# Kernel optimization log

Hardware: AMD Instinct MI355X
Metric: run time of the kernel (lower is better)

The kernel has to match this reference:

```python
import jax, jax.numpy as jnp
import numpy as np
from jax import lax

# Model dims (match init_kwargs / input_specs)
B, L, DIN, H = 8, 2048, 40, 128
NL, DSTATE, DCONV, EXPAND, DTRANK = 4, 16, 4, 2, 8
DINNER = EXPAND * H
NHOR, NCLS = 3, 3


def _layer_norm(x, g, b, eps=1e-5):
    m = jnp.mean(x, -1, keepdims=True)
    v = jnp.mean((x - m) ** 2, -1, keepdims=True)
    return (x - m) * lax.rsqrt(v + eps) * g + b


def _mamba_block(x, in_w, cw, cb, xp_w, dt_w, dt_b, A_log, Dp, out_w):
    # x: (b, l, H)
    b, l, _ = x.shape
    xz = x @ in_w.T                      # (b, l, 2*d_inner)
    xh, z = jnp.split(xz, 2, axis=-1)
    # causal depthwise conv1d (torch pads d_conv-1 both sides then slices [:l])
    xc = lax.conv_general_dilated(
        xh.transpose(0, 2, 1), cw, window_strides=(1,),
        padding=[(DCONV - 1, 0)], feature_group_count=DINNER,
        dimension_numbers=('NCH', 'OIH', 'NCH')) + cb[None, :, None]
    xh = jax.nn.silu(xc.transpose(0, 2, 1))   # (b, l, d_inner)
    # selective SSM
    A = -jnp.exp(A_log)                   # (N,)
    xp = xh @ xp_w.T                      # (b, l, dt_rank + 2N)
    dt_in, Bm, Cm = jnp.split(xp, [DTRANK, DTRANK + DSTATE], axis=-1)
    delta = jax.nn.softplus(dt_in @ dt_w.T + dt_b)          # (b, l, d_inner)
    dA = jnp.exp(delta[..., None] * A)                      # (b, l, d_inner, N)
    dBx = delta[..., None] * Bm[:, :, None, :] * xh[..., None]

    def step(h, inp):
        dA_t, dBx_t, C_t = inp
        h = dA_t * h + dBx_t              # (b, d_inner, N)
        y = jnp.einsum('bdn,bn->bd', h, C_t)
        return h, y

    h0 = jnp.zeros((b, DINNER, DSTATE), x.dtype)
    _, ys = lax.scan(step, h0, (dA.transpose(1, 0, 2, 3),
                                dBx.transpose(1, 0, 2, 3),
                                Cm.transpose(1, 0, 2)))
    y = ys.transpose(1, 0, 2) + Dp * xh   # (b, l, d_inner)
    y = y * jax.nn.silu(z)
    return y @ out_w.T                    # (b, l, H)


def _forward(x, input_proj_w, input_proj_b, input_norm_g, input_norm_b,
             norm_g, norm_b, in_proj_w, conv_w, conv_b, x_proj_w,
             dt_proj_w, dt_proj_b, A_log, D, out_proj_w,
             head_w1, head_b1, head_w2, head_b2):
    h = _layer_norm(x @ input_proj_w.T + input_proj_b, input_norm_g, input_norm_b)
    for i in range(NL):  # residual Mamba blocks (pre-norm)
        h = h + _mamba_block(_layer_norm(h, norm_g[i], norm_b[i]),
                             in_proj_w[i], conv_w[i], conv_b[i], x_proj_w[i],
                             dt_proj_w[i], dt_proj_b[i], A_log[i], D[i], out_proj_w[i])
    feats = h[:, -1, :]                   # last-timestep features (b, H)
    logits = []
    for i in range(NHOR):
        t = jax.nn.gelu(feats @ head_w1[i].T + head_b1[i], approximate=False)
        logits.append(t @ head_w2[i].T + head_b2[i])
    return jnp.stack(logits, axis=1)      # (b, num_horizons, num_classes)


def setup_inputs() -> dict:
    key = jax.random.key(0)
    ks = jax.random.split(key, 12)
    rn = lambda k, s, sc=0.02: jax.random.normal(k, s, jnp.float32) * sc
    A0 = jnp.log(jnp.arange(1, DSTATE + 1, dtype=jnp.float32))
    return {
        'x': jax.random.normal(ks[0], (B, L, DIN), jnp.float32),
        'input_proj_w': rn(ks[1], (H, DIN)),
        'input_proj_b': jnp.zeros((H,), jnp.float32),
        'input_norm_g': jnp.ones((H,), jnp.float32),
        'input_norm_b': jnp.zeros((H,), jnp.float32),
        'norm_g': jnp.ones((NL, H), jnp.float32),
        'norm_b': jnp.zeros((NL, H), jnp.float32),
        'in_proj_w': rn(ks[2], (NL, 2 * DINNER, H)),
        'conv_w': rn(ks[3], (NL, DINNER, 1, DCONV), 0.1),
        'conv_b': jnp.zeros((NL, DINNER), jnp.float32),
        'x_proj_w': rn(ks[4], (NL, DTRANK + 2 * DSTATE, DINNER)),
        'dt_proj_w': rn(ks[5], (NL, DINNER, DTRANK), 0.1),
        'dt_proj_b': rn(ks[6], (NL, DINNER), 0.1),
        'A_log': jnp.tile(A0, (NL, 1)),
        'D': jnp.ones((NL, DINNER), jnp.float32),
        'out_proj_w': rn(ks[7], (NL, H, DINNER)),
        'head_w1': rn(ks[8], (NHOR, H // 2, H)),
        'head_b1': jnp.zeros((NHOR, H // 2), jnp.float32),
        'head_w2': rn(ks[9], (NHOR, NCLS, H // 2)),
        'head_b2': jnp.zeros((NHOR, NCLS), jnp.float32),
    }


def reference(x, input_proj_w, input_proj_b, input_norm_g, input_norm_b,
              norm_g, norm_b, in_proj_w, conv_w, conv_b, x_proj_w,
              dt_proj_w, dt_proj_b, A_log, D, out_proj_w,
              head_w1, head_b1, head_w2, head_b2):
    return _forward(x, input_proj_w, input_proj_b, input_norm_g, input_norm_b,
                    norm_g, norm_b, in_proj_w, conv_w, conv_b, x_proj_w,
                    dt_proj_w, dt_proj_b, A_log, D, out_proj_w,
                    head_w1, head_b1, head_w2, head_b2)
```

## Files before the change

kernel.cpp:

```cpp
#include <hip/hip_runtime.h>
#include <hip/hip_bf16.h>
#include <math.h>

#define B_  8
#define L_  2048
#define DIN_ 40
#define H_  128
#define NL_ 4
#define DSTATE_ 16
#define DCONV_ 4
#define DTRANK_ 8
#define DINNER_ 256
#define NHOR_ 3
#define NCLS_ 3

#define CL_ 32
#define NC_ 64

__device__ __forceinline__ float softplus_f(float x) {
  return fmaxf(x, 0.f) + log1pf(__expf(-fabsf(x)));
}

__device__ __forceinline__ bool a_is_arith(const float* Ag, float& An0) {
  An0 = -__expf(Ag[0]);
  if (An0 == 0.f) return false;
  bool ok = true;
#pragma unroll
  for (int n = 1; n < DSTATE_; n++) {
    float r = -__expf(Ag[n]) / An0;
    ok = ok && (fabsf(r - (float)(n + 1)) < 1e-3f);
  }
  return ok;
}

__global__ __launch_bounds__(128) void k_in_ln(
    const float* __restrict__ x, const float* __restrict__ w,
    const float* __restrict__ bias, const float* __restrict__ g,
    const float* __restrict__ bb, float* __restrict__ hout)
{
  int row = blockIdx.x;
  int o = threadIdx.x;
  __shared__ float xs[DIN_];
  __shared__ float sm[4];
  if (o < DIN_) xs[o] = x[(size_t)row * DIN_ + o];
  __syncthreads();
  float acc = bias[o];
  const float* wr = w + (size_t)o * DIN_;
#pragma unroll
  for (int k = 0; k < DIN_; k++) acc += xs[k] * wr[k];
  float s = acc;
#pragma unroll
  for (int m = 32; m >= 1; m >>= 1) s += __shfl_xor(s, m);
  if ((o & 63) == 0) sm[o >> 6] = s;
  __syncthreads();
  float mean = (sm[0] + sm[1]) * (1.f / H_);
  float dv = acc - mean;
  float q = dv * dv;
#pragma unroll
  for (int m = 32; m >= 1; m >>= 1) q += __shfl_xor(q, m);
  if ((o & 63) == 0) sm[2 + (o >> 6)] = q;
  __syncthreads();
  float var = (sm[2] + sm[3]) * (1.f / H_);
  hout[(size_t)row * H_ + o] = dv * rsqrtf(var + 1e-5f) * g[o] + bb[o];
}

__global__ __launch_bounds__(128) void k_ln(
    const float* __restrict__ in, const float* __restrict__ g,
    const float* __restrict__ bb, float* __restrict__ out)
{
  int row = blockIdx.x;
  int o = threadIdx.x;
  float v = in[(size_t)row * H_ + o];
  __shared__ float sm[4];
  float s = v;
#pragma unroll
  for (int m = 32; m >= 1; m >>= 1) s += __shfl_xor(s, m);
  if ((o & 63) == 0) sm[o >> 6] = s;
  __syncthreads();
  float mean = (sm[0] + sm[1]) * (1.f / H_);
  float dv = v - mean;
  float q = dv * dv;
#pragma unroll
  for (int m = 32; m >= 1; m >>= 1) q += __shfl_xor(q, m);
  if ((o & 63) == 0) sm[2 + (o >> 6)] = q;
  __syncthreads();
  float var = (sm[2] + sm[3]) * (1.f / H_);
  out[(size_t)row * H_ + o] = dv * rsqrtf(var + 1e-5f) * g[o] + bb[o];
}

template <int BM, int BN, int EPI>
__global__ __launch_bounds__(256) void gemm_tn(
    const float* __restrict__ A, const float* __restrict__ Bw,
    float* __restrict__ C0, float* __restrict__ C1,
    int M, int N, int K)
{
  constexpr int TM = BM / 16, TN = BN / 16;
  __shared__ float As[16][BM + 4];
  __shared__ float Bs[16][BN + 4];
  const int tid = threadIdx.x;
  const int tx = tid & 15, ty = tid >> 4;
  const int bm0 = blockIdx.y * BM, bn0 = blockIdx.x * BN;
  float acc[TM][TN] = {};
  constexpr int AF4 = BM / 64;
  constexpr int BF4 = BN / 64;

  for (int k0 = 0; k0 < K; k0 += 16) {
#pragma unroll
    for (int i = 0; i < AF4; i++) {
      int f = tid + i * 256;
      int r = f >> 2, kq = (f & 3) << 2;
      float4 v = *reinterpret_cast<const float4*>(&A[(size_t)(bm0 + r) * K + k0 + kq]);
      As[kq + 0][r] = v.x; As[kq + 1][r] = v.y;
      As[kq + 2][r] = v.z; As[kq + 3][r] = v.w;
    }
#pragma unroll
    for (int i = 0; i < BF4; i++) {
      int f = tid + i * 256;
      int rn = f >> 2, kq = (f & 3) << 2;
      float4 v = make_float4(0.f, 0.f, 0.f, 0.f);
      if (bn0 + rn < N)
        v = *reinterpret_cast<const float4*>(&Bw[(size_t)(bn0 + rn) * K + k0 + kq]);
      Bs[kq + 0][rn] = v.x; Bs[kq + 1][rn] = v.y;
      Bs[kq + 2][rn] = v.z; Bs[kq + 3][rn] = v.w;
    }
    __syncthreads();
#pragma unroll
    for (int k = 0; k < 16; k++) {
      float a[TM], b[TN];
#pragma unroll
      for (int i = 0; i < TM; i += 4) {
        float4 v = *reinterpret_cast<const float4*>(&As[k][ty * TM + i]);
        a[i] = v.x; a[i + 1] = v.y; a[i + 2] = v.z; a[i + 3] = v.w;
      }
#pragma unroll
      for (int j = 0; j < TN; j += 4) {
        float4 v = *reinterpret_cast<const float4*>(&Bs[k][tx * TN + j]);
        b[j] = v.x; b[j + 1] = v.y; b[j + 2] = v.z; b[j + 3] = v.w;
      }
#pragma unroll
      for (int i = 0; i < TM; i++)
#pragma unroll
        for (int j = 0; j < TN; j++) acc[i][j] += a[i] * b[j];
    }
    __syncthreads();
  }

#pragma unroll
  for (int i = 0; i < TM; i++) {
    int r = bm0 + ty * TM + i;
    int c0 = bn0 + tx * TN;
    if (c0 >= N) continue;
    float4 v = make_float4(acc[i][0], acc[i][1], acc[i][2], acc[i][3]);
    if (EPI == 0) {
      *reinterpret_cast<float4*>(&C0[(size_t)r * N + c0]) = v;
    } else {
      if (c0 < 256) *reinterpret_cast<float4*>(&C0[(size_t)r * 256 + c0]) = v;
      else          *reinterpret_cast<float4*>(&C1[(size_t)r * 256 + (c0 - 256)]) = v;
    }
  }
}

template <bool DO_LN>
__global__ __launch_bounds__(256) void gemm_out(
    const float* __restrict__ A, const float* __restrict__ Bw,
    float* __restrict__ H, float* __restrict__ XN,
    const float* __restrict__ g, const float* __restrict__ bb)
{
  constexpr int BM = 64, BN = 128, K = DINNER_, N = H_;
  constexpr int TM = 4, TN = 8;
  __shared__ float As[16][BM + 4];
  __shared__ float Bs[16][BN + 4];
  const int tid = threadIdx.x;
  const int tx = tid & 15, ty = tid >> 4;
  const int bm0 = blockIdx.x * BM;
  float acc[TM][TN] = {};

  for (int k0 = 0; k0 < K; k0 += 16) {
    {
      int f = tid;
      int r = f >> 2, kq = (f & 3) << 2;
      float4 v = *reinterpret_cast<const float4*>(&A[(size_t)(bm0 + r) * K + k0 + kq]);
      As[kq + 0][r] = v.x; As[kq + 1][r] = v.y;
      As[kq + 2][r] = v.z; As[kq + 3][r] = v.w;
    }
#pragma unroll
    for (int i = 0; i < 2; i++) {
      int f = tid + i * 256;
      int rn = f >> 2, kq = (f & 3) << 2;
      float4 v = *reinterpret_cast<const float4*>(&Bw[(size_t)rn * K + k0 + kq]);
      Bs[kq + 0][rn] = v.x; Bs[kq + 1][rn] = v.y;
      Bs[kq + 2][rn] = v.z; Bs[kq + 3][rn] = v.w;
    }
    __syncthreads();
#pragma unroll
    for (int k = 0; k < 16; k++) {
      float a[TM], b[TN];
      float4 av = *reinterpret_cast<const float4*>(&As[k][ty * TM]);
      a[0] = av.x; a[1] = av.y; a[2] = av.z; a[3] = av.w;
#pragma unroll
      for (int j = 0; j < TN; j += 4) {
        float4 v = *reinterpret_cast<const float4*>(&Bs[k][tx * TN + j]);
        b[j] = v.x; b[j + 1] = v.y; b[j + 2] = v.z; b[j + 3] = v.w;
      }
#pragma unroll
      for (int i = 0; i < TM; i++)
#pragma unroll
        for (int j = 0; j < TN; j++) acc[i][j] += a[i] * b[j];
    }
    __syncthreads();
  }

  float gv[TN], bv[TN];
  if (DO_LN) {
#pragma unroll
    for (int j = 0; j < TN; j += 4) {
      float4 t = *reinterpret_cast<const float4*>(&g[tx * TN + j]);
      gv[j] = t.x; gv[j+1] = t.y; gv[j+2] = t.z; gv[j+3] = t.w;
      float4 u = *reinterpret_cast<const float4*>(&bb[tx * TN + j]);
      bv[j] = u.x; bv[j+1] = u.y; bv[j+2] = u.z; bv[j+3] = u.w;
    }
  }
#pragma unroll
  for (int i = 0; i < TM; i++) {
    int r = bm0 + ty * TM + i;
    float hv[TN];
#pragma unroll
    for (int j = 0; j < TN; j += 4) {
      float4 o = *reinterpret_cast<const float4*>(&H[(size_t)r * N + tx * TN + j]);
      hv[j]   = o.x + acc[i][j];
      hv[j+1] = o.y + acc[i][j+1];
      hv[j+2] = o.z + acc[i][j+2];
      hv[j+3] = o.w + acc[i][j+3];
    }
#pragma unroll
    for (int j = 0; j < TN; j += 4)
      *reinterpret_cast<float4*>(&H[(size_t)r * N + tx * TN + j]) =
          make_float4(hv[j], hv[j+1], hv[j+2], hv[j+3]);
    if (DO_LN) {
      float s = 0.f;
#pragma unroll
      for (int j = 0; j < TN; j++) s += hv[j];
#pragma unroll
      for (int m = 1; m < 16; m <<= 1) s += __shfl_xor(s, m);
      float mean = s * (1.f / N);
      float q = 0.f;
#pragma unroll
      for (int j = 0; j < TN; j++) { float d = hv[j] - mean; q += d * d; }
#pragma unroll
      for (int m = 1; m < 16; m <<= 1) q += __shfl_xor(q, m);
      float rstd = rsqrtf(q * (1.f / N) + 1e-5f);
      float xo[TN];
#pragma unroll
      for (int j = 0; j < TN; j++) xo[j] = (hv[j] - mean) * rstd * gv[j] + bv[j];
#pragma unroll
      for (int j = 0; j < TN; j += 4)
        *reinterpret_cast<float4*>(&XN[(size_t)r * N + tx * TN + j]) =
            make_float4(xo[j], xo[j+1], xo[j+2], xo[j+3]);
    }
  }
}

__global__ __launch_bounds__(256, 4) void k_front(
    const float* __restrict__ xx, const float* __restrict__ cw,
    const float* __restrict__ cb, const float* __restrict__ xpw,
    const float* __restrict__ dtw, const float* __restrict__ dtb,
    const float* __restrict__ Ag, const float* __restrict__ Dp,
    float* __restrict__ xpg, float* __restrict__ ylbuf,
    float* __restrict__ hf, float* __restrict__ ss)
{
  int b = blockIdx.x >> 6;
  int c = blockIdx.x & (NC_ - 1);
  int d = threadIdx.x;
  int row0 = b * L_ + c * CL_;

  __shared__ float xhs[CL_][256];
  __shared__ float xps[CL_ * 40];

  float w0 = cw[d * DCONV_ + 0], w1 = cw[d * DCONV_ + 1];
  float w2 = cw[d * DCONV_ + 2], w3 = cw[d * DCONV_ + 3];
  float cbv = cb[d];
  float xm3 = (c > 0) ? xx[(size_t)(row0 - 3) * 256 + d] : 0.f;
  float xm2 = (c > 0) ? xx[(size_t)(row0 - 2) * 256 + d] : 0.f;
  float xm1 = (c > 0) ? xx[(size_t)(row0 - 1) * 256 + d] : 0.f;
#pragma unroll
  for (int t = 0; t < CL_; t++) {
    float xc = xx[(size_t)(row0 + t) * 256 + d];
    float a = cbv + w0 * xm3 + w1 * xm2 + w2 * xm1 + w3 * xc;
    xhs[t][d] = a / (1.f + __expf(-a));
    xm3 = xm2; xm2 = xm1; xm1 = xc;
  }
  __syncthreads();

  for (int o = d; o < CL_ * 40; o += 256) {
    int t = o / 40, j = o - t * 40;
    const float* wrow = xpw + (size_t)j * 256;
    float av = 0.f;
#pragma unroll
    for (int k = 0; k < 256; k += 4) {
      float4 wv = *reinterpret_cast<const float4*>(&wrow[k]);
      float4 xv = *reinterpret_cast<const float4*>(&xhs[t][k]);
      av += xv.x * wv.x + xv.y * wv.y + xv.z * wv.z + xv.w * wv.w;
    }
    xps[o] = av;
    xpg[(size_t)row0 * 40 + o] = av;
  }
  __syncthreads();

  float dtw_r[DTRANK_];
#pragma unroll
  for (int k = 0; k < DTRANK_; k++) dtw_r[k] = dtw[d * DTRANK_ + k];
  float dtb_r = dtb[d];
  float Dv = Dp[d];
  float An0;
  bool fast = a_is_arith(Ag, An0);
  float h[DSTATE_] = {};
  float S = 0.f;
  size_t base = (size_t)row0 * 256 + d;
  if (fast) {
#pragma unroll
    for (int t = 0; t < CL_; t++) {
      float acc = dtb_r;
#pragma unroll
      for (int k = 0; k < DTRANK_; k++) acc += xps[t * 40 + k] * dtw_r[k];
      float dv = softplus_f(acc);
      float xv = xhs[t][d];
      S += dv;
      float dx = dv * xv;
      float E = __expf(dv * An0);
      float f = E, y = 0.f;
#pragma unroll
      for (int n = 0; n < DSTATE_; n++) {
        h[n] = f * h[n] + dx * xps[t * 40 + 8 + n];
        y += h[n] * xps[t * 40 + 24 + n];
        f *= E;
      }
      ylbuf[base + t * 256] = y + Dv * xv;
    }
  } else {
    for (int t = 0; t < CL_; t++) {
      float acc = dtb_r;
#pragma unroll
      for (int k = 0; k < DTRANK_; k++) acc += xps[t * 40 + k] * dtw_r[k];
      float dv = softplus_f(acc);
      float xv = xhs[t][d];
      S += dv;
      float dx = dv * xv;
      float y = 0.f;
      for (int n = 0; n < DSTATE_; n++) {
        float dA = __expf(dv * (-__expf(Ag[n])));
        h[n] = dA * h[n] + dx * xps[t * 40 + 8 + n];
        y += h[n] * xps[t * 40 + 24 + n];
      }
      ylbuf[base + t * 256] = y + Dv * xv;
    }
  }
  ss[(size_t)blockIdx.x * 256 + d] = S;
  float* hp = hf + ((size_t)blockIdx.x * 256 + d) * DSTATE_;
#pragma unroll
  for (int n = 0; n < DSTATE_; n += 4)
    *reinterpret_cast<float4*>(&hp[n]) = make_float4(h[n], h[n+1], h[n+2], h[n+3]);
}

__global__ __launch_bounds__(64) void k_scan2(
    const float* __restrict__ Ag, const float* __restrict__ ss,
    float* __restrict__ hf)
{
  int gid = blockIdx.x * 64 + threadIdx.x;
  int b = gid >> 12;
  int r = gid & 4095;
  int d = r >> 4;
  int n = r & 15;
  float An = -__expf(Ag[n]);
  float hi = 0.f;
  for (int ct = 0; ct < NC_ / 8; ct++) {
    float f[8], s[8];
#pragma unroll
    for (int j = 0; j < 8; j++) {
      int c = ct * 8 + j;
      f[j] = hf[((size_t)(b * NC_ + c) * 4096) + r];
      s[j] = ss[(size_t)(b * NC_ + c) * 256 + d];
    }
#pragma unroll
    for (int j = 0; j < 8; j++) {
      int c = ct * 8 + j;
      float P = __expf(An * s[j]);
      hf[((size_t)(b * NC_ + c) * 4096) + r] = hi;
      hi = P * hi + f[j];
    }
  }
}

__global__ __launch_bounds__(256, 4) void k_scan3(
    const float* __restrict__ xpg, const float* __restrict__ dtw,
    const float* __restrict__ dtb, const float* __restrict__ Ag,
    const float* __restrict__ hf, const float* __restrict__ ylbuf,
    float* zz)
{
  int b = blockIdx.x >> 6;
  int c = blockIdx.x & (NC_ - 1);
  int d = threadIdx.x;
  int row0 = b * L_ + c * CL_;
  __shared__ float xps[CL_ * 40];
  for (int i = d; i < CL_ * 40; i += 256) xps[i] = xpg[(size_t)row0 * 40 + i];
  float dtw_r[DTRANK_];
#pragma unroll
  for (int k = 0; k < DTRANK_; k++) dtw_r[k] = dtw[d * DTRANK_ + k];
  float dtb_r = dtb[d];
  float An0;
  bool fast = a_is_arith(Ag, An0);
  __syncthreads();
  float h0[DSTATE_];
  {
    const float* hp = hf + ((size_t)blockIdx.x * 256 + d) * DSTATE_;
#pragma unroll
    for (int n = 0; n < DSTATE_; n += 4) {
      float4 v = *reinterpret_cast<const float4*>(&hp[n]);
      h0[n] = v.x; h0[n+1] = v.y; h0[n+2] = v.z; h0[n+3] = v.w;
    }
  }
  size_t base = (size_t)row0 * 256 + d;
  float cd = 0.f;
  if (fast) {
#pragma unroll
    for (int t = 0; t < CL_; t++) {
      float acc = dtb_r;
#pragma unroll
      for (int k = 0; k < DTRANK_; k++) acc += xps[t * 40 + k] * dtw_r[k];
      cd += softplus_f(acc);
      float E = __expf(cd * An0);
      float p = E, corr = 0.f;
#pragma unroll
      for (int n = 0; n < DSTATE_; n++) {
        corr += p * h0[n] * xps[t * 40 + 24 + n];
        p *= E;
      }
      float yv = ylbuf[base + t * 256] + corr;
      float zv = zz[base + t * 256];
      zz[base + t * 256] = yv * (zv / (1.f + __expf(-zv)));
    }
  } else {
    for (int t = 0; t < CL_; t++) {
      float acc = dtb_r;
#pragma unroll
      for (int k = 0; k < DTRANK_; k++) acc += xps[t * 40 + k] * dtw_r[k];
      cd += softplus_f(acc);
      float corr = 0.f;
      for (int n = 0; n < DSTATE_; n++)
        corr += __expf(cd * (-__expf(Ag[n]))) * h0[n] * xps[t * 40 + 24 + n];
      float yv = ylbuf[base + t * 256] + corr;
      float zv = zz[base + t * 256];
      zz[base + t * 256] = yv * (zv / (1.f + __expf(-zv)));
    }
  }
}

__global__ __launch_bounds__(64) void k_heads(
    const float* __restrict__ hbuf, const float* __restrict__ w1,
    const float* __restrict__ b1, const float* __restrict__ w2,
    const float* __restrict__ b2, float* __restrict__ out)
{
  int hor = blockIdx.x, b = blockIdx.y;
  int j = threadIdx.x;
  __shared__ float fs[H_];
  __shared__ float ts[64];
  const float* fr = hbuf + ((size_t)b * L_ + (L_ - 1)) * H_;
  fs[j] = fr[j];
  fs[j + 64] = fr[j + 64];
  __syncthreads();
  float acc = b1[hor * 64 + j];
  const float* wr = w1 + (size_t)(hor * 64 + j) * H_;
#pragma unroll
  for (int k = 0; k < H_; k++) acc += fs[k] * wr[k];
  ts[j] = 0.5f * acc * (1.f + erff(acc * 0.70710678118654752f));
  __syncthreads();
  if (j < NCLS_) {
    float a2 = b2[hor * NCLS_ + j];
    const float* w2r = w2 + (size_t)(hor * NCLS_ + j) * 64;
    float s = a2;
#pragma unroll
    for (int k = 0; k < 64; k++) s += ts[k] * w2r[k];
    out[(size_t)b * (NHOR_ * NCLS_) + hor * NCLS_ + j] = s;
  }
}

extern "C" void kernel_launch(void* const* d_in, const int* in_sizes, int n_in,
                              void* d_out, int out_size, void* d_ws, size_t ws_size,
                              hipStream_t stream)
{
  const float* x            = (const float*)d_in[0];
  const float* input_proj_w = (const float*)d_in[1];
  const float* input_proj_b = (const float*)d_in[2];
  const float* input_norm_g = (const float*)d_in[3];
  const float* input_norm_b = (const float*)d_in[4];
  const float* norm_g       = (const float*)d_in[5];
  const float* norm_b       = (const float*)d_in[6];
  const float* in_proj_w    = (const float*)d_in[7];
  const float* conv_w       = (const float*)d_in[8];
  const float* conv_b       = (const float*)d_in[9];
  const float* x_proj_w     = (const float*)d_in[10];
  const float* dt_proj_w    = (const float*)d_in[11];
  const float* dt_proj_b    = (const float*)d_in[12];
  const float* A_log        = (const float*)d_in[13];
  const float* Dp           = (const float*)d_in[14];
  const float* out_proj_w   = (const float*)d_in[15];
  const float* head_w1      = (const float*)d_in[16];
  const float* head_b1      = (const float*)d_in[17];
  const float* head_w2      = (const float*)d_in[18];
  const float* head_b2      = (const float*)d_in[19];
  float* out = (float*)d_out;

  const int ROWS = B_ * L_;
  float* ws = (float*)d_ws;
  float* h     = ws;
  float* xn    = h  + (size_t)ROWS * H_;
  float* xx    = xn + (size_t)ROWS * H_;
  float* zz    = xx + (size_t)ROWS * 256;
  float* ylbuf = zz + (size_t)ROWS * 256;
  float* xp    = ylbuf + (size_t)ROWS * 256;
  float* ss    = xp + (size_t)ROWS * 40;
  float* hf    = xn;

  k_in_ln<<<ROWS, 128, 0, stream>>>(x, input_proj_w, input_proj_b,
                                    input_norm_g, input_norm_b, h);
  k_ln<<<ROWS, 128, 0, stream>>>(h, norm_g, norm_b, xn);

  for (int l = 0; l < NL_; l++) {
    gemm_tn<128, 64, 2><<<dim3(512 / 64, ROWS / 128), 256, 0, stream>>>(
        xn, in_proj_w + (size_t)l * 512 * H_, xx, zz, ROWS, 512, H_);
    k_front<<<B_ * NC_, 256, 0, stream>>>(
        xx, conv_w + (size_t)l * DINNER_ * DCONV_, conv_b + (size_t)l * DINNER_,
        x_proj_w + (size_t)l * 40 * DINNER_,
        dt_proj_w + (size_t)l * DINNER_ * DTRANK_, dt_proj_b + (size_t)l * DINNER_,
        A_log + l * DSTATE_, Dp + (size_t)l * DINNER_,
        xp, ylbuf, hf, ss);
    k_scan2<<<(B_ * DINNER_ * DSTATE_) / 64, 64, 0, stream>>>(A_log + l * DSTATE_, ss, hf);
    k_scan3<<<B_ * NC_, 256, 0, stream>>>(
        xp, dt_proj_w + (size_t)l * DINNER_ * DTRANK_, dt_proj_b + (size_t)l * DINNER_,
        A_log + l * DSTATE_, hf, ylbuf, zz);
    if (l < NL_ - 1) {
      gemm_out<true><<<ROWS / 64, 256, 0, stream>>>(
          zz, out_proj_w + (size_t)l * H_ * DINNER_, h, xn,
          norm_g + (l + 1) * H_, norm_b + (l + 1) * H_);
    } else {
      gemm_out<false><<<ROWS / 64, 256, 0, stream>>>(
          zz, out_proj_w + (size_t)l * H_ * DINNER_, h, nullptr, nullptr, nullptr);
    }
  }

  k_heads<<<dim3(NHOR_, B_), 64, 0, stream>>>(h, head_w1, head_b1, head_w2, head_b2, out);
}
```

Before: 933.8 us.

## Halve scan chunk length, use log-depth power chain, widen in_proj GEMM tile

Changes the chunked selective scan from 64 chunks of 32 steps to 128 chunks of 16 steps. This doubles the number of blocks for the front and correction kernels and shortens each sequential chain, at the cost of a longer inter-chunk scan in k_scan2 and more chunk-state traffic. The serial E^n multiply chain is replaced by a tree-structured power computation to cut dependency latency. The xhs shared array is padded, the hf buffer is moved out of xn into its own region now that it is larger, and the in_proj GEMM uses a 128-wide N tile with a looped float4 epilogue.

```diff
diff --git a/kernel.cpp b/kernel.cpp
--- a/kernel.cpp
+++ b/kernel.cpp
@@ -14,8 +14,8 @@
 #define NHOR_ 3
 #define NCLS_ 3
 
-#define CL_ 32
-#define NC_ 64
+#define CL_ 16
+#define NC_ 128
 
 __device__ __forceinline__ float softplus_f(float x) {
   return fmaxf(x, 0.f) + log1pf(__expf(-fabsf(x)));
@@ -31,6 +31,14 @@
     ok = ok && (fabsf(r - (float)(n + 1)) < 1e-3f);
   }
   return ok;
+}
+
+__device__ __forceinline__ void pow_chain16(float E, float* f_) {
+  float E2 = E * E, E4 = E2 * E2, E8 = E4 * E4;
+  f_[0] = E;        f_[1] = E2;        f_[2] = E2 * E;    f_[3] = E4;
+  f_[4] = E4 * E;   f_[5] = E4 * E2;   f_[6] = f_[5] * E; f_[7] = E8;
+  f_[8] = E8 * E;   f_[9] = E8 * E2;   f_[10] = f_[9] * E; f_[11] = E8 * E4;
+  f_[12] = f_[11] * E; f_[13] = f_[11] * E2; f_[14] = f_[13] * E; f_[15] = E8 * E8;
 }
 
 __global__ __launch_bounds__(128) void k_in_ln(
@@ -148,14 +156,17 @@
 #pragma unroll
   for (int i = 0; i < TM; i++) {
     int r = bm0 + ty * TM + i;
-    int c0 = bn0 + tx * TN;
-    if (c0 >= N) continue;
-    float4 v = make_float4(acc[i][0], acc[i][1], acc[i][2], acc[i][3]);
-    if (EPI == 0) {
-      *reinterpret_cast<float4*>(&C0[(size_t)r * N + c0]) = v;
-    } else {
-      if (c0 < 256) *reinterpret_cast<float4*>(&C0[(size_t)r * 256 + c0]) = v;
-      else          *reinterpret_cast<float4*>(&C1[(size_t)r * 256 + (c0 - 256)]) = v;
+#pragma unroll
+    for (int jj = 0; jj < TN; jj += 4) {
+      int c0 = bn0 + tx * TN + jj;
+      if (c0 >= N) continue;
+      float4 v = make_float4(acc[i][jj], acc[i][jj+1], acc[i][jj+2], acc[i][jj+3]);
+      if (EPI == 0) {
+        *reinterpret_cast<float4*>(&C0[(size_t)r * N + c0]) = v;
+      } else {
+        if (c0 < 256) *reinterpret_cast<float4*>(&C0[(size_t)r * 256 + c0]) = v;
+        else          *reinterpret_cast<float4*>(&C1[(size_t)r * 256 + (c0 - 256)]) = v;
+      }
     }
   }
 }
@@ -260,20 +271,20 @@
   }
 }
 
-__global__ __launch_bounds__(256, 4) void k_front(
+__global__ __launch_bounds__(256, 4) void k_front2(
     const float* __restrict__ xx, const float* __restrict__ cw,
     const float* __restrict__ cb, const float* __restrict__ xpw,
     const float* __restrict__ dtw, const float* __restrict__ dtb,
     const float* __restrict__ Ag, const float* __restrict__ Dp,
-    float* __restrict__ xpg, float* __restrict__ ylbuf,
+    float* __restrict__ xpg, float* __restrict__ yl,
     float* __restrict__ hf, float* __restrict__ ss)
 {
-  int b = blockIdx.x >> 6;
+  int b = blockIdx.x >> 7;
   int c = blockIdx.x & (NC_ - 1);
   int d = threadIdx.x;
   int row0 = b * L_ + c * CL_;
 
-  __shared__ float xhs[CL_][256];
+  __shared__ float xhs[CL_][260];
   __shared__ float xps[CL_ * 40];
 
   float w0 = cw[d * DCONV_ + 0], w1 = cw[d * DCONV_ + 1];
@@ -327,14 +338,15 @@
       S += dv;
       float dx = dv * xv;
       float E = __expf(dv * An0);
-      float f = E, y = 0.f;
+      float f_[DSTATE_];
+      pow_chain16(E, f_);
+      float y = 0.f;
 #pragma unroll
       for (int n = 0; n < DSTATE_; n++) {
-        h[n] = f * h[n] + dx * xps[t * 40 + 8 + n];
+        h[n] = f_[n] * h[n] + dx * xps[t * 40 + 8 + n];
         y += h[n] * xps[t * 40 + 24 + n];
-        f *= E;
       }
-      ylbuf[base + t * 256] = y + Dv * xv;
+      yl[base + t * 256] = y + Dv * xv;
     }
   } else {
     for (int t = 0; t < CL_; t++) {
@@ -351,7 +363,7 @@
         h[n] = dA * h[n] + dx * xps[t * 40 + 8 + n];
         y += h[n] * xps[t * 40 + 24 + n];
       }
-      ylbuf[base + t * 256] = y + Dv * xv;
+      yl[base + t * 256] = y + Dv * xv;
     }
   }
   ss[(size_t)blockIdx.x * 256 + d] = S;
@@ -390,13 +402,13 @@
   }
 }
 
-__global__ __launch_bounds__(256, 4) void k_scan3(
+__global__ __launch_bounds__(256, 4) void k_scan3c(
     const float* __restrict__ xpg, const float* __restrict__ dtw,
     const float* __restrict__ dtb, const float* __restrict__ Ag,
-    const float* __restrict__ hf, const float* __restrict__ ylbuf,
+    const float* __restrict__ hf, const float* __restrict__ yl,
     float* zz)
 {
-  int b = blockIdx.x >> 6;
+  int b = blockIdx.x >> 7;
   int c = blockIdx.x & (NC_ - 1);
   int d = threadIdx.x;
   int row0 = b * L_ + c * CL_;
@@ -428,13 +440,13 @@
       for (int k = 0; k < DTRANK_; k++) acc += xps[t * 40 + k] * dtw_r[k];
       cd += softplus_f(acc);
       float E = __expf(cd * An0);
-      float p = E, corr = 0.f;
-#pragma unroll
-      for (int n = 0; n < DSTATE_; n++) {
-        corr += p * h0[n] * xps[t * 40 + 24 + n];
-        p *= E;
-      }
-      float yv = ylbuf[base + t * 256] + corr;
+      float p_[DSTATE_];
+      pow_chain16(E, p_);
+      float corr = 0.f;
+#pragma unroll
+      for (int n = 0; n < DSTATE_; n++)
+        corr += p_[n] * h0[n] * xps[t * 40 + 24 + n];
+      float yv = yl[base + t * 256] + corr;
       float zv = zz[base + t * 256];
       zz[base + t * 256] = yv * (zv / (1.f + __expf(-zv)));
     }
@@ -447,7 +459,7 @@
       float corr = 0.f;
       for (int n = 0; n < DSTATE_; n++)
         corr += __expf(cd * (-__expf(Ag[n]))) * h0[n] * xps[t * 40 + 24 + n];
-      float yv = ylbuf[base + t * 256] + corr;
+      float yv = yl[base + t * 256] + corr;
       float zv = zz[base + t * 256];
       zz[base + t * 256] = yv * (zv / (1.f + __expf(-zv)));
     }
@@ -511,32 +523,32 @@
 
   const int ROWS = B_ * L_;
   float* ws = (float*)d_ws;
-  float* h     = ws;
-  float* xn    = h  + (size_t)ROWS * H_;
-  float* xx    = xn + (size_t)ROWS * H_;
-  float* zz    = xx + (size_t)ROWS * 256;
-  float* ylbuf = zz + (size_t)ROWS * 256;
-  float* xp    = ylbuf + (size_t)ROWS * 256;
-  float* ss    = xp + (size_t)ROWS * 40;
-  float* hf    = xn;
+  float* h    = ws;
+  float* xn   = h  + (size_t)ROWS * H_;
+  float* xx   = xn + (size_t)ROWS * H_;
+  float* zz   = xx + (size_t)ROWS * 256;
+  float* yl   = zz + (size_t)ROWS * 256;
+  float* xp   = yl + (size_t)ROWS * 256;
+  float* ss   = xp + (size_t)ROWS * 40;
+  float* hf   = ss + (size_t)(B_ * NC_) * 256;
 
   k_in_ln<<<ROWS, 128, 0, stream>>>(x, input_proj_w, input_proj_b,
                                     input_norm_g, input_norm_b, h);
   k_ln<<<ROWS, 128, 0, stream>>>(h, norm_g, norm_b, xn);
 
   for (int l = 0; l < NL_; l++) {
-    gemm_tn<128, 64, 2><<<dim3(512 / 64, ROWS / 128), 256, 0, stream>>>(
+    gemm_tn<128, 128, 2><<<dim3(512 / 128, ROWS / 128), 256, 0, stream>>>(
         xn, in_proj_w + (size_t)l * 512 * H_, xx, zz, ROWS, 512, H_);
-    k_front<<<B_ * NC_, 256, 0, stream>>>(
+    k_front2<<<B_ * NC_, 256, 0, stream>>>(
         xx, conv_w + (size_t)l * DINNER_ * DCONV_, conv_b + (size_t)l * DINNER_,
         x_proj_w + (size_t)l * 40 * DINNER_,
         dt_proj_w + (size_t)l * DINNER_ * DTRANK_, dt_proj_b + (size_t)l * DINNER_,
         A_log + l * DSTATE_, Dp + (size_t)l * DINNER_,
-        xp, ylbuf, hf, ss);
+        xp, yl, hf, ss);
     k_scan2<<<(B_ * DINNER_ * DSTATE_) / 64, 64, 0, stream>>>(A_log + l * DSTATE_, ss, hf);
-    k_scan3<<<B_ * NC_, 256, 0, stream>>>(
+    k_scan3c<<<B_ * NC_, 256, 0, stream>>>(
         xp, dt_proj_w + (size_t)l * DINNER_ * DTRANK_, dt_proj_b + (size_t)l * DINNER_,
-        A_log + l * DSTATE_, hf, ylbuf, zz);
+        A_log + l * DSTATE_, hf, yl, zz);
     if (l < NL_ - 1) {
       gemm_out<true><<<ROWS / 64, 256, 0, stream>>>(
           zz, out_proj_w + (size_t)l * H_ * DINNER_, h, xn,
```

Result: slower. 976.5 us (+4.6%).
